# Kernel optimization log

Hardware: AMD Instinct MI355X
Metric: run time of the kernel (lower is better)

The kernel has to match this reference:

```python
import jax, jax.numpy as jnp
import numpy as np

N = 100000
E = 3200000
IN_CH, HID, OUT = 256, 64, 32


def setup_inputs() -> dict:
    key = jax.random.key(0)
    ks = jax.random.split(key, 8)
    x = jax.random.normal(ks[0], (N, IN_CH), dtype=jnp.float32)
    edge_index = jax.random.randint(ks[1], (2, E), 0, N, dtype=jnp.int64)
    # Glorot-ish init for weights, zeros for biases (PyG GCNConv: lin has no bias; conv bias added post-aggregation)
    W1 = jax.random.normal(ks[2], (IN_CH, HID), dtype=jnp.float32) / np.sqrt(IN_CH)
    b1 = jnp.zeros((HID,), dtype=jnp.float32)
    W2 = jax.random.normal(ks[3], (HID, OUT), dtype=jnp.float32) / np.sqrt(HID)
    b2 = jnp.zeros((OUT,), dtype=jnp.float32)
    Wc = jax.random.normal(ks[4], (OUT, 1), dtype=jnp.float32) / np.sqrt(OUT)
    bc = jnp.zeros((1,), dtype=jnp.float32)
    return {"x": x, "edge_index": edge_index, "W1": W1, "b1": b1,
            "W2": W2, "b2": b2, "Wc": Wc, "bc": bc}


def _gcn_norm(edge_index, num_nodes):
    # Add self-loops (PyG default), compute symmetric normalization D^{-1/2} A D^{-1/2}
    loops = jnp.arange(num_nodes, dtype=edge_index.dtype)
    row = jnp.concatenate([edge_index[0], loops])  # source
    col = jnp.concatenate([edge_index[1], loops])  # target (aggregation index)
    ones = jnp.ones(row.shape[0], dtype=jnp.float32)
    deg = jax.ops.segment_sum(ones, col, num_segments=num_nodes)
    dis = jnp.where(deg > 0, jax.lax.rsqrt(jnp.maximum(deg, 1e-12)), 0.0)
    norm = dis[row] * dis[col]  # [E+N]
    return row, col, norm


def _gcn_conv(x, W, b, row, col, norm, num_nodes):
    h = x @ W                                   # [N, F_out] dense transform first
    msg = h[row] * norm[:, None]                # gather + scale per edge
    agg = jax.ops.segment_sum(msg, col, num_segments=num_nodes)
    return agg + b


def reference(x, edge_index, W1, b1, W2, b2, Wc, bc):
    num_nodes = x.shape[0]
    row, col, norm = _gcn_norm(edge_index, num_nodes)
    h = jax.nn.elu(_gcn_conv(x, W1, b1, row, col, norm, num_nodes))
    h = jax.nn.elu(_gcn_conv(h, W2, b2, row, col, norm, num_nodes))
    return (h @ Wc + bc)[:, 0]                  # squeeze(1) -> [N]
```

## Files before the change

### kernel.cpp

```cpp
#include <hip/hip_runtime.h>
#include <hip/hip_fp16.h>
#include <math.h>

#define N_NODES 100000
#define N_EDGES 3200000
#define IN_CH   256
#define HID     64
#define OUTC    32
#define NBUCK   ((N_NODES + 127) / 128)
#define CHUNK   8192
#define CAP     4608

static constexpr size_t align256(size_t x) { return (x + 255) & ~(size_t)255; }
static constexpr size_t OFF_PTRB = 0;
static constexpr size_t OFF_PTRE = OFF_PTRB + align256((size_t)N_NODES * 4);
static constexpr size_t OFF_GCUR = OFF_PTRE + align256((size_t)N_NODES * 4);
static constexpr size_t OFF_DIS  = OFF_GCUR + align256((size_t)NBUCK * 4);
static constexpr size_t OFF_SRC  = OFF_DIS  + align256((size_t)N_NODES * 4);
static constexpr size_t OFF_PART = OFF_SRC  + align256((size_t)NBUCK * CAP * 4);
static constexpr size_t OFF_S1   = OFF_PART;
static constexpr size_t OFF_S2   = OFF_PART + align256((size_t)NBUCK * CAP * 4);

typedef _Float16 f16;
typedef f16 f16x8 __attribute__((ext_vector_type(8)));
typedef float f32x4 __attribute__((ext_vector_type(4)));

__device__ __forceinline__ void acc8(float* acc, float4 raw) {
    const __half2* hp = (const __half2*)&raw;
    float2 f0 = __half22float2(hp[0]);
    float2 f1 = __half22float2(hp[1]);
    float2 f2 = __half22float2(hp[2]);
    float2 f3 = __half22float2(hp[3]);
    acc[0] += f0.x; acc[1] += f0.y; acc[2] += f1.x; acc[3] += f1.y;
    acc[4] += f2.x; acc[5] += f2.y; acc[6] += f3.x; acc[7] += f3.y;
}

__global__ __launch_bounds__(256) void bucket_init(int* __restrict__ gcur) {
    int b = blockIdx.x * 256 + threadIdx.x;
    if (b < NBUCK) gcur[b] = b * CAP;
}

__global__ __launch_bounds__(256) void partition_edges(const int* __restrict__ row,
                                                       const int* __restrict__ col,
                                                       int* __restrict__ gcur,
                                                       int* __restrict__ part) {
    __shared__ int lhist[NBUCK];
    __shared__ int lbase[NBUCK];
    __shared__ int lcur[NBUCK];
    const int t  = threadIdx.x;
    const int e0 = blockIdx.x * CHUNK;
    const int e1 = (e0 + CHUNK < N_EDGES) ? (e0 + CHUNK) : N_EDGES;
    for (int i = t; i < NBUCK; i += 256) lhist[i] = 0;
    __syncthreads();

    for (int e = e0 + t; e < e1; e += 256)
        atomicAdd(&lhist[col[e] >> 7], 1);
    __syncthreads();

    const int off = (int)((blockIdx.x * 131u) % NBUCK);
    for (int i = t; i < NBUCK; i += 256) {
        int bb = i + off;
        if (bb >= NBUCK) bb -= NBUCK;
        int c = lhist[bb];
        lbase[bb] = (c > 0) ? atomicAdd(&gcur[bb], c) : 0;
        lcur[bb] = 0;
    }
    __syncthreads();

    for (int e = e0 + t; e < e1; e += 256) {
        int d = col[e];
        int b = d >> 7;
        int r = atomicAdd(&lcur[b], 1);
        part[lbase[b] + r] = row[e] | ((d & 127) << 17);
    }
}

__global__ __launch_bounds__(256) void bucket_build(const int* __restrict__ gcur,
                                                    const int* __restrict__ part,
                                                    int* __restrict__ ptrb,
                                                    int* __restrict__ ptre,
                                                    float* __restrict__ dis,
                                                    int* __restrict__ srcs) {
    __shared__ int pcache[CAP];
    __shared__ int lh[128];
    __shared__ int lb[128];
    __shared__ int lcur[128];
    __shared__ int ls[128];
    const int b = blockIdx.x;
    const int t = threadIdx.x;
    if (t < 128) { lh[t] = 0; lcur[t] = 0; }
    __syncthreads();
    const int cnt = gcur[b] - b * CAP;
    const size_t pbase = (size_t)b * CAP;

    for (int i = t; i < cnt; i += 256) {
        int p = part[pbase + i];
        pcache[i] = p;
        atomicAdd(&lh[p >> 17], 1);
    }
    __syncthreads();

    int val = (t < 128) ? lh[t] : 0;
    if (t < 128) ls[t] = val;
    __syncthreads();
    for (int off = 1; off < 128; off <<= 1) {
        int add = (t >= off && t < 128) ? ls[t - off] : 0;
        __syncthreads();
        if (t < 128) ls[t] += add;
        __syncthreads();
    }
    if (t < 128) lb[t] = ls[t] - val;
    __syncthreads();

    int v = b * 128 + t;
    if (t < 128 && v < N_NODES) {
        ptrb[v] = b * CAP + lb[t];
        ptre[v] = b * CAP + lb[t] + val;
        dis[v]  = rsqrtf((float)val + 1.0f);
    }

    for (int i = t; i < cnt; i += 256) {
        int p    = pcache[i];
        int dlow = p >> 17;
        int src  = p & 0x1FFFF;
        int r    = atomicAdd(&lcur[dlow], 1);
        srcs[pbase + lb[dlow] + r] = src;
    }
}

__global__ __launch_bounds__(256) void gemm1(const float* __restrict__ x,
                                             const float* __restrict__ W1,
                                             const float* __restrict__ dis,
                                             __half* __restrict__ s1h) {
    __shared__ __align__(16) char lds_raw[30720];
    f16* xh  = (f16*)lds_raw;
    f16* xl  = (f16*)(lds_raw + 10240);
    f16* wth = (f16*)(lds_raw + 20480);
    f16* wtl = (f16*)(lds_raw + 25600);

    const int t    = threadIdx.x;
    const int row0 = blockIdx.x * 128;
    const int lane = t & 63;
    const int wv   = t >> 6;
    const int lr   = lane & 15;
    const int kg   = lane >> 4;

    f32x4 acc[2][4];
#pragma unroll
    for (int m = 0; m < 2; ++m)
#pragma unroll
        for (int n = 0; n < 4; ++n) acc[m][n] = (f32x4){0.f, 0.f, 0.f, 0.f};

    for (int kt = 0; kt < 8; ++kt) {
#pragma unroll
        for (int i = 0; i < 4; ++i) {
            int L  = i * 256 + t;
            int r  = L >> 3;
            int k4 = L & 7;
            int rg = row0 + r;
            float4 v = make_float4(0.f, 0.f, 0.f, 0.f);
            if (rg < N_NODES)
                v = ((const float4*)x)[(size_t)rg * 64 + kt * 8 + k4];
            union { f16 h[4]; unsigned long long u; } ph, pl;
            const float* vf = (const float*)&v;
#pragma unroll
            for (int c = 0; c < 4; ++c) {
                f16 hi = (f16)vf[c];
                ph.h[c] = hi;
                pl.h[c] = (f16)(vf[c] - (float)hi);
            }
            *(unsigned long long*)(&xh[r * 40 + k4 * 4]) = ph.u;
            *(unsigned long long*)(&xl[r * 40 + k4 * 4]) = pl.u;
        }
#pragma unroll
        for (int i = 0; i < 2; ++i) {
            int L  = i * 256 + t;
            int k  = L >> 4;
            int j4 = L & 15;
            float4 v = ((const float4*)W1)[(size_t)(kt * 32 + k) * 16 + j4];
            const float* vf = (const float*)&v;
#pragma unroll
            for (int c = 0; c < 4; ++c) {
                f16 hi = (f16)vf[c];
                wth[(j4 * 4 + c) * 40 + k] = hi;
                wtl[(j4 * 4 + c) * 40 + k] = (f16)(vf[c] - (float)hi);
            }
        }
        __syncthreads();

        f16x8 ah[2], al[2], bh[4], bl[4];
#pragma unroll
        for (int m = 0; m < 2; ++m) {
            ah[m] = *(const f16x8*)(&xh[(wv * 32 + m * 16 + lr) * 40 + kg * 8]);
            al[m] = *(const f16x8*)(&xl[(wv * 32 + m * 16 + lr) * 40 + kg * 8]);
        }
#pragma unroll
        for (int n = 0; n < 4; ++n) {
            bh[n] = *(const f16x8*)(&wth[(n * 16 + lr) * 40 + kg * 8]);
            bl[n] = *(const f16x8*)(&wtl[(n * 16 + lr) * 40 + kg * 8]);
        }
#pragma unroll
        for (int m = 0; m < 2; ++m)
#pragma unroll
            for (int n = 0; n < 4; ++n) {
                acc[m][n] = __builtin_amdgcn_mfma_f32_16x16x32_f16(ah[m], bh[n], acc[m][n], 0, 0, 0);
                acc[m][n] = __builtin_amdgcn_mfma_f32_16x16x32_f16(ah[m], bl[n], acc[m][n], 0, 0, 0);
                acc[m][n] = __builtin_amdgcn_mfma_f32_16x16x32_f16(al[m], bh[n], acc[m][n], 0, 0, 0);
            }
        __syncthreads();
    }

    f16* ob = (f16*)lds_raw;
#pragma unroll
    for (int m = 0; m < 2; ++m) {
#pragma unroll
        for (int r = 0; r < 4; ++r) {
            int rl = wv * 32 + m * 16 + kg * 4 + r;
            int rg = row0 + rl;
            float d = dis[rg < N_NODES ? rg : (N_NODES - 1)];
#pragma unroll
            for (int n = 0; n < 4; ++n)
                ob[rl * 72 + n * 16 + lr] = (f16)(acc[m][n][r] * d);
        }
    }
    __syncthreads();
#pragma unroll
    for (int i = 0; i < 4; ++i) {
        int L = i * 256 + t;
        int r = L >> 3;
        int sg = L & 7;
        int rg = row0 + r;
        if (rg < N_NODES) {
            f16x8 v = *(const f16x8*)(&ob[r * 72 + sg * 8]);
            *(f16x8*)(s1h + (size_t)rg * HID + sg * 8) = v;
        }
    }
}

__global__ __launch_bounds__(256) void gather1(const __half* __restrict__ s1h,
                                               const int* __restrict__ ptrb,
                                               const int* __restrict__ ptre,
                                               const int* __restrict__ srcs,
                                               const float* __restrict__ dis,
                                               const float* __restrict__ b1,
                                               const float* __restrict__ W2,
                                               __half* __restrict__ s2h) {
    __shared__ float w2lds[HID * OUTC];
    __shared__ float hbuf[4][HID];

    const int t = threadIdx.x;
    {
        float4* l4 = (float4*)w2lds;
        const float4* s4 = (const float4*)W2;
        l4[t] = s4[t];
        l4[256 + t] = s4[256 + t];
    }
    __syncthreads();

    const int j = t & 63;
    const int w = t >> 6;
    const int l = j & 31;
    const int h = j >> 5;
    const int v = __builtin_amdgcn_readfirstlane(blockIdx.x * 4 + w);
    const __half2* s12 = (const __half2*)s1h;

    float2 acc;
    {
        float2 self = __half22float2(s12[(v << 5) | l]);
        acc = (h == 0) ? self : make_float2(0.f, 0.f);
    }
    const int beg = ptrb[v];
    const int end = ptre[v];

    for (int base = beg; base < end; base += 64) {
        int mysrc = 0;
        if (base + j < end) mysrc = srcs[base + j];
        int nk = end - base;
        if (nk > 64) nk = 64;
        const int full = nk >> 1;
        int i = 0;
        for (; i + 8 <= full; i += 8) {
            int s  = 2 * i + h;
            int a0 = __shfl(mysrc, s,      64);
            int a1 = __shfl(mysrc, s + 2,  64);
            int a2 = __shfl(mysrc, s + 4,  64);
            int a3 = __shfl(mysrc, s + 6,  64);
            int a4 = __shfl(mysrc, s + 8,  64);
            int a5 = __shfl(mysrc, s + 10, 64);
            int a6 = __shfl(mysrc, s + 12, 64);
            int a7 = __shfl(mysrc, s + 14, 64);
            float2 g0 = __half22float2(s12[(a0 << 5) | l]);
            float2 g1 = __half22float2(s12[(a1 << 5) | l]);
            float2 g2 = __half22float2(s12[(a2 << 5) | l]);
            float2 g3 = __half22float2(s12[(a3 << 5) | l]);
            float2 g4 = __half22float2(s12[(a4 << 5) | l]);
            float2 g5 = __half22float2(s12[(a5 << 5) | l]);
            float2 g6 = __half22float2(s12[(a6 << 5) | l]);
            float2 g7 = __half22float2(s12[(a7 << 5) | l]);
            acc.x += ((g0.x + g1.x) + (g2.x + g3.x)) + ((g4.x + g5.x) + (g6.x + g7.x));
            acc.y += ((g0.y + g1.y) + (g2.y + g3.y)) + ((g4.y + g5.y) + (g6.y + g7.y));
        }
        if (2 * i < nk) {
            const int last = nk - 1;
#pragma unroll
            for (int u = 0; u < 8; ++u) {
                int s  = 2 * (i + u) + h;
                int sc = s < last ? s : last;
                int a  = __shfl(mysrc, sc, 64);
                float wgt = (s < nk) ? 1.f : 0.f;
                float2 g = __half22float2(s12[(a << 5) | l]);
                acc.x = fmaf(wgt, g.x, acc.x);
                acc.y = fmaf(wgt, g.y, acc.y);
            }
        }
    }
    acc.x += __shfl_xor(acc.x, 32, 64);
    acc.y += __shfl_xor(acc.y, 32, 64);

    float dv = dis[v];
    float2 bb = *(const float2*)(b1 + 2 * l);
    float t0 = dv * acc.x + bb.x;
    float t1 = dv * acc.y + bb.y;
    float h0 = t0 > 0.f ? t0 : (expf(t0) - 1.f);
    float h1 = t1 > 0.f ? t1 : (expf(t1) - 1.f);
    if (h == 0) {
        hbuf[w][2 * l]     = h0;
        hbuf[w][2 * l + 1] = h1;
    }

    const int jo = j & 31;
    const int kb = (j >> 5) * 32;
    float p = 0.f;
#pragma unroll
    for (int kk = 0; kk < 32; ++kk)
        p += hbuf[w][kb + kk] * w2lds[(kb + kk) * OUTC + jo];
    p += __shfl_xor(p, 32, 64);
    if (j < 32) {
        s2h[(size_t)v * OUTC + jo] = __float2half(dv * p);
    }
}

__global__ __launch_bounds__(256) void gather2(const __half* __restrict__ s2h,
                                               const int* __restrict__ ptrb,
                                               const int* __restrict__ ptre,
                                               const int* __restrict__ srcs,
                                               const float* __restrict__ dis,
                                               const float* __restrict__ b2,
                                               const float* __restrict__ Wc,
                                               const float* __restrict__ bc,
                                               float* __restrict__ out) {
    const int j = threadIdx.x & 63;
    const int w = threadIdx.x >> 6;
    const int l = j & 3;
    const int e = j >> 2;
    const int v = __builtin_amdgcn_readfirstlane(blockIdx.x * 4 + w);
    const float4* s24 = (const float4*)s2h;

    float acc[8] = {0.f, 0.f, 0.f, 0.f, 0.f, 0.f, 0.f, 0.f};
    if (e == 0) acc8(acc, s24[(v << 2) | l]);

    const int beg = ptrb[v];
    const int end = ptre[v];
    for (int base = beg; base < end; base += 64) {
        int mys = 0;
        if (base + j < end) mys = srcs[base + j];
        int nk = end - base;
        if (nk > 64) nk = 64;
        int off = 0;
        for (; off + 32 <= nk; off += 32) {
            int a0 = __shfl(mys, off + e,      64);
            int a1 = __shfl(mys, off + 16 + e, 64);
            float4 r0 = s24[(a0 << 2) | l];
            float4 r1 = s24[(a1 << 2) | l];
            acc8(acc, r0);
            acc8(acc, r1);
        }
        if (off < nk) {
            const int last = nk - 1;
            int s0 = off + e, s1 = off + 16 + e;
            int a0 = __shfl(mys, s0 < last ? s0 : last, 64);
            int a1 = __shfl(mys, s1 < last ? s1 : last, 64);
            if (s0 < nk) acc8(acc, s24[(a0 << 2) | l]);
            if (s1 < nk) acc8(acc, s24[(a1 << 2) | l]);
        }
    }
#pragma unroll
    for (int i = 0; i < 8; ++i) {
        acc[i] += __shfl_xor(acc[i], 4, 64);
        acc[i] += __shfl_xor(acc[i], 8, 64);
        acc[i] += __shfl_xor(acc[i], 16, 64);
        acc[i] += __shfl_xor(acc[i], 32, 64);
    }

    float dv = dis[v];
    float4 ba = ((const float4*)b2)[2 * l];
    float4 bb = ((const float4*)b2)[2 * l + 1];
    float4 wa = ((const float4*)Wc)[2 * l];
    float4 wb = ((const float4*)Wc)[2 * l + 1];
    const float* bf = (const float*)&ba;
    const float* bg = (const float*)&bb;
    const float* wf = (const float*)&wa;
    const float* wg = (const float*)&wb;
    float p = 0.f;
#pragma unroll
    for (int i = 0; i < 8; ++i) {
        float bias = (i < 4) ? bf[i] : bg[i - 4];
        float wc   = (i < 4) ? wf[i] : wg[i - 4];
        float tt = dv * acc[i] + bias;
        float hh = tt > 0.f ? tt : (expf(tt) - 1.f);
        p += hh * wc;
    }
    p += __shfl_xor(p, 1, 64);
    p += __shfl_xor(p, 2, 64);
    if (j == 0) out[v] = p + bc[0];
}

extern "C" void kernel_launch(void* const* d_in, const int* in_sizes, int n_in,
                              void* d_out, int out_size, void* d_ws, size_t ws_size,
                              hipStream_t stream) {
    const float* x  = (const float*)d_in[0];
    const int*   ei = (const int*)d_in[1];
    const float* W1 = (const float*)d_in[2];
    const float* b1 = (const float*)d_in[3];
    const float* W2 = (const float*)d_in[4];
    const float* b2 = (const float*)d_in[5];
    const float* Wc = (const float*)d_in[6];
    const float* bc = (const float*)d_in[7];
    float* out = (float*)d_out;

    const int* row = ei;
    const int* col = ei + N_EDGES;

    char* ws = (char*)d_ws;
    int*    ptrb = (int*)   (ws + OFF_PTRB);
    int*    ptre = (int*)   (ws + OFF_PTRE);
    int*    gcur = (int*)   (ws + OFF_GCUR);
    float*  dis  = (float*) (ws + OFF_DIS);
    int*    srcs = (int*)   (ws + OFF_SRC);
    int*    part = (int*)   (ws + OFF_PART);
    __half* s1h  = (__half*)(ws + OFF_S1);
    __half* s2h  = (__half*)(ws + OFF_S2);

    bucket_init    <<<(NBUCK + 255) / 256, 256, 0, stream>>>(gcur);
    partition_edges<<<(N_EDGES + CHUNK - 1) / CHUNK, 256, 0, stream>>>(row, col, gcur, part);
    bucket_build   <<<NBUCK, 256, 0, stream>>>(gcur, part, ptrb, ptre, dis, srcs);

    gemm1  <<<(N_NODES + 127) / 128, 256, 0, stream>>>(x, W1, dis, s1h);
    gather1<<<N_NODES / 4, 256, 0, stream>>>(s1h, ptrb, ptre, srcs, dis, b1, W2, s2h);
    gather2<<<N_NODES / 4, 256, 0, stream>>>(s2h, ptrb, ptre, srcs, dis, b2, Wc, bc, out);
}
```

Before: 401.9 us.

## Replace bucketed two-pass edge partition with global atomic counting sort CSR build

Swaps the LDS-bucketed partition plus per-bucket local sort for a plain CSR build: a global atomic degree histogram, a three-kernel prefix scan, and an atomic scatter of source indices. It removes the intermediate partition buffer and the fixed per-bucket capacity. In exchange it relies on 3.2M contended global atomics and random scattered writes, and it launches more kernels. Neighbour order within each node also becomes nondeterministic.

```diff
diff --git a/kernel.cpp b/kernel.cpp
--- a/kernel.cpp
+++ b/kernel.cpp
@@ -7,19 +7,18 @@
 #define IN_CH   256
 #define HID     64
 #define OUTC    32
-#define NBUCK   ((N_NODES + 127) / 128)
-#define CHUNK   8192
-#define CAP     4608
+#define NSCB    ((N_NODES + 1023) / 1024)
 
 static constexpr size_t align256(size_t x) { return (x + 255) & ~(size_t)255; }
 static constexpr size_t OFF_PTRB = 0;
 static constexpr size_t OFF_PTRE = OFF_PTRB + align256((size_t)N_NODES * 4);
-static constexpr size_t OFF_GCUR = OFF_PTRE + align256((size_t)N_NODES * 4);
-static constexpr size_t OFF_DIS  = OFF_GCUR + align256((size_t)NBUCK * 4);
-static constexpr size_t OFF_SRC  = OFF_DIS  + align256((size_t)N_NODES * 4);
-static constexpr size_t OFF_PART = OFF_SRC  + align256((size_t)NBUCK * CAP * 4);
-static constexpr size_t OFF_S1   = OFF_PART;
-static constexpr size_t OFF_S2   = OFF_PART + align256((size_t)NBUCK * CAP * 4);
+static constexpr size_t OFF_CUR  = OFF_PTRE + align256((size_t)N_NODES * 4);
+static constexpr size_t OFF_DEG  = OFF_CUR  + align256((size_t)N_NODES * 4);
+static constexpr size_t OFF_DIS  = OFF_DEG  + align256((size_t)N_NODES * 4);
+static constexpr size_t OFF_SUMS = OFF_DIS  + align256((size_t)N_NODES * 4);
+static constexpr size_t OFF_SRC  = OFF_SUMS + align256((size_t)128 * 4);
+static constexpr size_t OFF_S1   = OFF_SRC  + align256((size_t)N_EDGES * 4);
+static constexpr size_t OFF_S2   = OFF_S1   + align256((size_t)N_NODES * HID * 2);
 
 typedef _Float16 f16;
 typedef f16 f16x8 __attribute__((ext_vector_type(8)));
@@ -35,96 +34,78 @@
     acc[4] += f2.x; acc[5] += f2.y; acc[6] += f3.x; acc[7] += f3.y;
 }
 
-__global__ __launch_bounds__(256) void bucket_init(int* __restrict__ gcur) {
-    int b = blockIdx.x * 256 + threadIdx.x;
-    if (b < NBUCK) gcur[b] = b * CAP;
-}
-
-__global__ __launch_bounds__(256) void partition_edges(const int* __restrict__ row,
-                                                       const int* __restrict__ col,
-                                                       int* __restrict__ gcur,
-                                                       int* __restrict__ part) {
-    __shared__ int lhist[NBUCK];
-    __shared__ int lbase[NBUCK];
-    __shared__ int lcur[NBUCK];
-    const int t  = threadIdx.x;
-    const int e0 = blockIdx.x * CHUNK;
-    const int e1 = (e0 + CHUNK < N_EDGES) ? (e0 + CHUNK) : N_EDGES;
-    for (int i = t; i < NBUCK; i += 256) lhist[i] = 0;
+__global__ __launch_bounds__(256) void k_zero(int* __restrict__ deg) {
+    int g = blockIdx.x * 256 + threadIdx.x;
+    if (g < N_NODES) deg[g] = 0;
+}
+
+__global__ __launch_bounds__(256) void k_hist(const int* __restrict__ col,
+                                              int* __restrict__ deg) {
+    const int stride = gridDim.x * 256;
+    for (int e = blockIdx.x * 256 + threadIdx.x; e < N_EDGES; e += stride)
+        atomicAdd(&deg[col[e]], 1);
+}
+
+__global__ __launch_bounds__(1024) void k_scan1(const int* __restrict__ deg,
+                                                int* __restrict__ ptrb,
+                                                int* __restrict__ sums) {
+    __shared__ int ls[1024];
+    const int t = threadIdx.x;
+    const int g = blockIdx.x * 1024 + t;
+    int v = (g < N_NODES) ? deg[g] : 0;
+    ls[t] = v;
     __syncthreads();
-
-    for (int e = e0 + t; e < e1; e += 256)
-        atomicAdd(&lhist[col[e] >> 7], 1);
-    __syncthreads();
-
-    const int off = (int)((blockIdx.x * 131u) % NBUCK);
-    for (int i = t; i < NBUCK; i += 256) {
-        int bb = i + off;
-        if (bb >= NBUCK) bb -= NBUCK;
-        int c = lhist[bb];
-        lbase[bb] = (c > 0) ? atomicAdd(&gcur[bb], c) : 0;
-        lcur[bb] = 0;
-    }
-    __syncthreads();
-
-    for (int e = e0 + t; e < e1; e += 256) {
-        int d = col[e];
-        int b = d >> 7;
-        int r = atomicAdd(&lcur[b], 1);
-        part[lbase[b] + r] = row[e] | ((d & 127) << 17);
-    }
-}
-
-__global__ __launch_bounds__(256) void bucket_build(const int* __restrict__ gcur,
-                                                    const int* __restrict__ part,
-                                                    int* __restrict__ ptrb,
-                                                    int* __restrict__ ptre,
-                                                    float* __restrict__ dis,
-                                                    int* __restrict__ srcs) {
-    __shared__ int pcache[CAP];
-    __shared__ int lh[128];
-    __shared__ int lb[128];
-    __shared__ int lcur[128];
+    for (int off = 1; off < 1024; off <<= 1) {
+        int add = (t >= off) ? ls[t - off] : 0;
+        __syncthreads();
+        ls[t] += add;
+        __syncthreads();
+    }
+    if (g < N_NODES) ptrb[g] = ls[t] - v;
+    if (t == 1023) sums[blockIdx.x] = ls[1023];
+}
+
+__global__ __launch_bounds__(128) void k_scan2(int* __restrict__ sums) {
     __shared__ int ls[128];
-    const int b = blockIdx.x;
     const int t = threadIdx.x;
-    if (t < 128) { lh[t] = 0; lcur[t] = 0; }
-    __syncthreads();
-    const int cnt = gcur[b] - b * CAP;
-    const size_t pbase = (size_t)b * CAP;
-
-    for (int i = t; i < cnt; i += 256) {
-        int p = part[pbase + i];
-        pcache[i] = p;
-        atomicAdd(&lh[p >> 17], 1);
-    }
-    __syncthreads();
-
-    int val = (t < 128) ? lh[t] : 0;
-    if (t < 128) ls[t] = val;
+    int v = (t < NSCB) ? sums[t] : 0;
+    ls[t] = v;
     __syncthreads();
     for (int off = 1; off < 128; off <<= 1) {
-        int add = (t >= off && t < 128) ? ls[t - off] : 0;
-        __syncthreads();
-        if (t < 128) ls[t] += add;
-        __syncthreads();
-    }
-    if (t < 128) lb[t] = ls[t] - val;
-    __syncthreads();
-
-    int v = b * 128 + t;
-    if (t < 128 && v < N_NODES) {
-        ptrb[v] = b * CAP + lb[t];
-        ptre[v] = b * CAP + lb[t] + val;
-        dis[v]  = rsqrtf((float)val + 1.0f);
-    }
-
-    for (int i = t; i < cnt; i += 256) {
-        int p    = pcache[i];
-        int dlow = p >> 17;
-        int src  = p & 0x1FFFF;
-        int r    = atomicAdd(&lcur[dlow], 1);
-        srcs[pbase + lb[dlow] + r] = src;
+        int add = (t >= off) ? ls[t - off] : 0;
+        __syncthreads();
+        ls[t] += add;
+        __syncthreads();
+    }
+    if (t < NSCB) sums[t] = ls[t] - v;
+}
+
+__global__ __launch_bounds__(1024) void k_scan3(const int* __restrict__ deg,
+                                                int* __restrict__ ptrb,
+                                                int* __restrict__ ptre,
+                                                int* __restrict__ cur,
+                                                float* __restrict__ dis,
+                                                const int* __restrict__ sums) {
+    const int g = blockIdx.x * 1024 + threadIdx.x;
+    if (g < N_NODES) {
+        int b = ptrb[g] + sums[blockIdx.x];
+        int d = deg[g];
+        ptrb[g] = b;
+        ptre[g] = b + d;
+        cur[g]  = b;
+        dis[g]  = rsqrtf((float)d + 1.0f);
+    }
+}
+
+__global__ __launch_bounds__(256) void k_scatter(const int* __restrict__ row,
+                                                 const int* __restrict__ col,
+                                                 int* __restrict__ cur,
+                                                 int* __restrict__ srcs) {
+    const int stride = gridDim.x * 256;
+    for (int e = blockIdx.x * 256 + threadIdx.x; e < N_EDGES; e += stride) {
+        int d = col[e];
+        int p = atomicAdd(&cur[d], 1);
+        srcs[p] = row[e];
     }
 }
 
@@ -434,16 +415,20 @@
     char* ws = (char*)d_ws;
     int*    ptrb = (int*)   (ws + OFF_PTRB);
     int*    ptre = (int*)   (ws + OFF_PTRE);
-    int*    gcur = (int*)   (ws + OFF_GCUR);
+    int*    cur  = (int*)   (ws + OFF_CUR);
+    int*    deg  = (int*)   (ws + OFF_DEG);
     float*  dis  = (float*) (ws + OFF_DIS);
+    int*    sums = (int*)   (ws + OFF_SUMS);
     int*    srcs = (int*)   (ws + OFF_SRC);
-    int*    part = (int*)   (ws + OFF_PART);
     __half* s1h  = (__half*)(ws + OFF_S1);
     __half* s2h  = (__half*)(ws + OFF_S2);
 
-    bucket_init    <<<(NBUCK + 255) / 256, 256, 0, stream>>>(gcur);
-    partition_edges<<<(N_EDGES + CHUNK - 1) / CHUNK, 256, 0, stream>>>(row, col, gcur, part);
-    bucket_build   <<<NBUCK, 256, 0, stream>>>(gcur, part, ptrb, ptre, dis, srcs);
+    k_zero   <<<(N_NODES + 255) / 256, 256, 0, stream>>>(deg);
+    k_hist   <<<1024, 256, 0, stream>>>(col, deg);
+    k_scan1  <<<NSCB, 1024, 0, stream>>>(deg, ptrb, sums);
+    k_scan2  <<<1, 128, 0, stream>>>(sums);
+    k_scan3  <<<NSCB, 1024, 0, stream>>>(deg, ptrb, ptre, cur, dis, sums);
+    k_scatter<<<2048, 256, 0, stream>>>(row, col, cur, srcs);
 
     gemm1  <<<(N_NODES + 127) / 128, 256, 0, stream>>>(x, W1, dis, s1h);
     gather1<<<N_NODES / 4, 256, 0, stream>>>(s1h, ptrb, ptre, srcs, dis, b1, W2, s2h);
```

After: 724.4 us. 1.8x slower.
